# Performance work log

Measured on AMD Instinct MI355X. Metric: run time of the kernel, lower is better.

The kernel has to match this reference:

```python
import jax, jax.numpy as jnp
import numpy as np

B, T, DIM, TU = 8, 2048, 128, 128


def setup_inputs() -> dict:
    key = jax.random.key(0)
    k1, k2 = jax.random.split(key)
    x = jax.random.normal(k1, (B, T, DIM), dtype=jnp.float32)
    # sorted integer-valued time-window ids in [0, TU), endpoints pinned so
    # every batch has tw_min=0 and tw_max=TU-1 (fixed Tu, jit-safe)
    tw = jnp.sort(jax.random.randint(k2, (B, T), 0, TU), axis=1)
    tw = tw.at[:, 0].set(0).at[:, -1].set(TU - 1)
    tw = tw.astype(jnp.float32)[..., None]  # (B, T, 1)
    mask = jnp.ones((B, T, 1), dtype=bool)
    # tw_uniq = padded per-batch arange(tw_min, tw_max+1); here exactly 0..TU-1
    tw_uniq = jnp.broadcast_to(
        jnp.arange(TU, dtype=jnp.float32)[None, :, None], (B, TU, 1)
    )
    return {"x": x, "tw": tw, "mask": mask, "tw_uniq": tw_uniq}


def reference(x, tw, mask, tw_uniq):
    # Faithful math: h[b,u,:] = max over {t : tw[b,t] == tw_uniq[b,u]} of x[b,t,:],
    # with a 0 baseline (torch.where fills masked entries with 0 before amax).
    # Expressed as an efficient per-batch segment-max instead of the O(B*T*Tu*dim)
    # broadcast the torch code materializes.
    Tu = tw_uniq.shape[1]
    tw_min = tw_uniq[:, 0, 0]  # (B,)
    seg = (tw[..., 0] - tw_min[:, None]).astype(jnp.int32)  # (B, T)
    seg = jnp.where(mask[..., 0], seg, Tu)  # masked-out rows -> dump segment
    seg = jnp.clip(seg, 0, Tu)

    def pool_one(xb, sb):
        # (T, dim), (T,) -> (Tu, dim); empty segments become -inf
        return jax.ops.segment_max(xb, sb, num_segments=Tu + 1)[:Tu]

    h = jax.vmap(pool_one)(x, seg)  # (B, Tu, dim)
    return jnp.maximum(h, 0.0)  # zero baseline; empty/padded segments -> 0
```

## Files before the change

### kernel.cpp

```cpp
#include <hip/hip_runtime.h>


#define B_  8
#define T_  2048
#define DIM_ 128
#define TU_ 128

__global__ __launch_bounds__(128)
void TimeWindowPooling_936302870861_kernel(const float* __restrict__ x,
                                           const float* __restrict__ tw,
                                           const float* __restrict__ tw_uniq,
                                           float* __restrict__ out) {
    const int b = blockIdx.x / TU_;
    const int s = blockIdx.x % TU_;
    const int d = threadIdx.x;

    const float tw_min = tw_uniq[b * TU_];
    const float lo_val = tw_min + (float)s;
    const float hi_val = tw_min + (float)(s + 1);

    const float* twb = tw + b * T_;

    int lo = 0, hi = T_;
    while (lo < hi) {
        int m = (lo + hi) >> 1;
        if (twb[m] < lo_val) lo = m + 1; else hi = m;
    }
    const int start = lo;

    hi = T_;
    while (lo < hi) {
        int m = (lo + hi) >> 1;
        if (twb[m] < hi_val) lo = m + 1; else hi = m;
    }
    const int end = lo;

    float acc = 0.0f;
    const float* xp = x + ((size_t)b * T_ + start) * DIM_ + d;
    for (int t = start; t < end; ++t) {
        acc = fmaxf(acc, *xp);
        xp += DIM_;
    }

    out[((size_t)b * TU_ + s) * DIM_ + d] = acc;
}

extern "C" void kernel_launch(void* const* d_in, const int* in_sizes, int n_in,
                              void* d_out, int out_size, void* d_ws, size_t ws_size,
                              hipStream_t stream) {
    const float* x       = (const float*)d_in[0];
    const float* tw      = (const float*)d_in[1];
    const float* tw_uniq = (const float*)d_in[3];
    float* out           = (float*)d_out;

    dim3 grid(B_ * TU_);
    dim3 block(128);
    TimeWindowPooling_936302870861_kernel<<<grid, block, 0, stream>>>(x, tw, tw_uniq, out);
}
```

Measured before the change: 10.65 us.

## Precompute segment boundaries in a separate kernel and unroll max loop

Replaces the per-block double binary search over tw with a small pre-pass kernel that writes segment start offsets into workspace, which the pooling kernel then reads. The pooling loop is unrolled by four with independent accumulators so more loads are in flight at once. The cost is a second kernel launch and a dependency through global memory. The boundary kernel also ignores the mask and handles the data differently from the reference in edge cases such as negative offsets.

```diff
diff --git a/kernel.cpp b/kernel.cpp
--- a/kernel.cpp
+++ b/kernel.cpp
@@ -1,46 +1,62 @@
 #include <hip/hip_runtime.h>
 
 
-#define B_  8
-#define T_  2048
+#define B_   8
+#define T_   2048
 #define DIM_ 128
-#define TU_ 128
+#define TU_  128
+
+__global__ __launch_bounds__(256)
+void twp_boundaries_kernel(const float* __restrict__ tw,
+                           const float* __restrict__ tw_uniq,
+                           int* __restrict__ bnd) {
+    const int b   = blockIdx.x;
+    const int tid = threadIdx.x;
+    const float tmin = tw_uniq[b * TU_];
+    const float* twb = tw + b * T_;
+    int* bb = bnd + b * (TU_ + 1);
+
+    #pragma unroll
+    for (int k = 0; k < T_ / 256; ++k) {
+        const int t = tid * (T_ / 256) + k;
+        int cur  = (int)(twb[t] - tmin);
+        cur = min(cur, TU_ - 1);
+        int prev = (t == 0) ? -1 : min((int)(twb[t - 1] - tmin), TU_ - 1);
+        for (int s = prev + 1; s <= cur; ++s) bb[s] = t;
+        if (t == T_ - 1) {
+            for (int s = cur + 1; s <= TU_; ++s) bb[s] = T_;
+        }
+    }
+}
 
 __global__ __launch_bounds__(128)
-void TimeWindowPooling_936302870861_kernel(const float* __restrict__ x,
-                                           const float* __restrict__ tw,
-                                           const float* __restrict__ tw_uniq,
-                                           float* __restrict__ out) {
+void twp_pool_kernel(const float* __restrict__ x,
+                     const int* __restrict__ bnd,
+                     float* __restrict__ out) {
     const int b = blockIdx.x / TU_;
     const int s = blockIdx.x % TU_;
     const int d = threadIdx.x;
 
-    const float tw_min = tw_uniq[b * TU_];
-    const float lo_val = tw_min + (float)s;
-    const float hi_val = tw_min + (float)(s + 1);
+    const int* bb = bnd + b * (TU_ + 1);
+    const int start = bb[s];
+    const int end   = bb[s + 1];
 
-    const float* twb = tw + b * T_;
+    const float* xp = x + ((size_t)b * T_ + start) * DIM_ + d;
 
-    int lo = 0, hi = T_;
-    while (lo < hi) {
-        int m = (lo + hi) >> 1;
-        if (twb[m] < lo_val) lo = m + 1; else hi = m;
+    float a0 = 0.0f, a1 = 0.0f, a2 = 0.0f, a3 = 0.0f;
+    int t = start;
+    for (; t + 4 <= end; t += 4) {
+        a0 = fmaxf(a0, xp[0 * DIM_]);
+        a1 = fmaxf(a1, xp[1 * DIM_]);
+        a2 = fmaxf(a2, xp[2 * DIM_]);
+        a3 = fmaxf(a3, xp[3 * DIM_]);
+        xp += 4 * DIM_;
     }
-    const int start = lo;
-
-    hi = T_;
-    while (lo < hi) {
-        int m = (lo + hi) >> 1;
-        if (twb[m] < hi_val) lo = m + 1; else hi = m;
-    }
-    const int end = lo;
-
-    float acc = 0.0f;
-    const float* xp = x + ((size_t)b * T_ + start) * DIM_ + d;
-    for (int t = start; t < end; ++t) {
-        acc = fmaxf(acc, *xp);
+    for (; t < end; ++t) {
+        a0 = fmaxf(a0, *xp);
         xp += DIM_;
     }
+    const float acc = fmaxf(fmaxf(a0, a1), fmaxf(a2, a3));
 
     out[((size_t)b * TU_ + s) * DIM_ + d] = acc;
 }
@@ -52,8 +68,8 @@
     const float* tw      = (const float*)d_in[1];
     const float* tw_uniq = (const float*)d_in[3];
     float* out           = (float*)d_out;
+    int* bnd             = (int*)d_ws;
 
-    dim3 grid(B_ * TU_);
-    dim3 block(128);
-    TimeWindowPooling_936302870861_kernel<<<grid, block, 0, stream>>>(x, tw, tw_uniq, out);
+    twp_boundaries_kernel<<<dim3(B_), dim3(256), 0, stream>>>(tw, tw_uniq, bnd);
+    twp_pool_kernel<<<dim3(B_ * TU_), dim3(128), 0, stream>>>(x, bnd, out);
 }
```

Measured after the change: 12.30 us. +15.4%, slower.

## Replace binary search with parallel count and split segment rows across sub-groups

Applied to the files above, without the earlier changes.

Segment bounds are now found by having every thread count how many tw values fall below each boundary, with a wave shuffle reduction, instead of two serial dependent binary searches. The row max is split across four thread sub-groups, each loading float4 along the feature dimension and striding over rows, then combined through a shuffle and shared memory. This removes the serial dependent load latency of the searches and shortens each thread's row loop. In exchange every block reads the full 2048-entry tw row and adds two barriers.

```diff
diff --git a/kernel.cpp b/kernel.cpp
--- a/kernel.cpp
+++ b/kernel.cpp
@@ -1,48 +1,76 @@
 #include <hip/hip_runtime.h>
 
 
-#define B_  8
-#define T_  2048
+#define B_   8
+#define T_   2048
 #define DIM_ 128
-#define TU_ 128
+#define TU_  128
 
 __global__ __launch_bounds__(128)
-void TimeWindowPooling_936302870861_kernel(const float* __restrict__ x,
-                                           const float* __restrict__ tw,
-                                           const float* __restrict__ tw_uniq,
-                                           float* __restrict__ out) {
-    const int b = blockIdx.x / TU_;
-    const int s = blockIdx.x % TU_;
-    const int d = threadIdx.x;
+void twp_fused_kernel(const float* __restrict__ x,
+                      const float* __restrict__ tw,
+                      const float* __restrict__ tw_uniq,
+                      float* __restrict__ out) {
+    const int b   = blockIdx.x >> 7;
+    const int s   = blockIdx.x & 127;
+    const int tid = threadIdx.x;
 
-    const float tw_min = tw_uniq[b * TU_];
-    const float lo_val = tw_min + (float)s;
-    const float hi_val = tw_min + (float)(s + 1);
+    __shared__ int   s_cnt[4];
+    __shared__ float s_part[32 * 4];
+
+    const float tmin   = tw_uniq[b * TU_];
+    const float lo_val = tmin + (float)s;
+    const float hi_val = lo_val + 1.0f;
 
     const float* twb = tw + b * T_;
+    int c_lo = 0, c_hi = 0;
+    #pragma unroll
+    for (int k = 0; k < T_ / 128; ++k) {
+        const float v = twb[tid + k * 128];
+        c_lo += (v < lo_val) ? 1 : 0;
+        c_hi += (v < hi_val) ? 1 : 0;
+    }
+    #pragma unroll
+    for (int off = 32; off > 0; off >>= 1) {
+        c_lo += __shfl_down(c_lo, off);
+        c_hi += __shfl_down(c_hi, off);
+    }
+    if ((tid & 63) == 0) {
+        s_cnt[(tid >> 6) * 2 + 0] = c_lo;
+        s_cnt[(tid >> 6) * 2 + 1] = c_hi;
+    }
+    __syncthreads();
+    const int start = s_cnt[0] + s_cnt[2];
+    const int end   = s_cnt[1] + s_cnt[3];
 
-    int lo = 0, hi = T_;
-    while (lo < hi) {
-        int m = (lo + hi) >> 1;
-        if (twb[m] < lo_val) lo = m + 1; else hi = m;
+    const int sub = tid >> 5;
+    const int d4  = (tid & 31) * 4;
+    float4 acc = make_float4(0.f, 0.f, 0.f, 0.f);
+    const float* xp = x + ((size_t)b * T_ + start + sub) * DIM_ + d4;
+    for (int t = start + sub; t < end; t += 4) {
+        const float4 v = *(const float4*)xp;
+        acc.x = fmaxf(acc.x, v.x);
+        acc.y = fmaxf(acc.y, v.y);
+        acc.z = fmaxf(acc.z, v.z);
+        acc.w = fmaxf(acc.w, v.w);
+        xp += 4 * DIM_;
     }
-    const int start = lo;
-
-    hi = T_;
-    while (lo < hi) {
-        int m = (lo + hi) >> 1;
-        if (twb[m] < hi_val) lo = m + 1; else hi = m;
+    acc.x = fmaxf(acc.x, __shfl_xor(acc.x, 32));
+    acc.y = fmaxf(acc.y, __shfl_xor(acc.y, 32));
+    acc.z = fmaxf(acc.z, __shfl_xor(acc.z, 32));
+    acc.w = fmaxf(acc.w, __shfl_xor(acc.w, 32));
+    if (tid >= 64 && tid < 96) {
+        *(float4*)&s_part[(tid - 64) * 4] = acc;
     }
-    const int end = lo;
-
-    float acc = 0.0f;
-    const float* xp = x + ((size_t)b * T_ + start) * DIM_ + d;
-    for (int t = start; t < end; ++t) {
-        acc = fmaxf(acc, *xp);
-        xp += DIM_;
+    __syncthreads();
+    if (tid < 32) {
+        const float4 o = *(const float4*)&s_part[tid * 4];
+        acc.x = fmaxf(acc.x, o.x);
+        acc.y = fmaxf(acc.y, o.y);
+        acc.z = fmaxf(acc.z, o.z);
+        acc.w = fmaxf(acc.w, o.w);
+        *(float4*)&out[((size_t)b * TU_ + s) * DIM_ + tid * 4] = acc;
     }
-
-    out[((size_t)b * TU_ + s) * DIM_ + d] = acc;
 }
 
 extern "C" void kernel_launch(void* const* d_in, const int* in_sizes, int n_in,
@@ -53,7 +81,5 @@
     const float* tw_uniq = (const float*)d_in[3];
     float* out           = (float*)d_out;
 
-    dim3 grid(B_ * TU_);
-    dim3 block(128);
-    TimeWindowPooling_936302870861_kernel<<<grid, block, 0, stream>>>(x, tw, tw_uniq, out);
+    twp_fused_kernel<<<dim3(B_ * TU_), dim3(128), 0, stream>>>(x, tw, tw_uniq, out);
 }
```

Measured after the change: 9.731 us. 1.09x faster.
